# Optimization experiments

Hardware: AMD Instinct MI355X
Metric: run time of the kernel (lower is better)

## Reference

```python
import math
import jax, jax.numpy as jnp
import numpy as np

FILTER_ORDER = 64
FILTER_EMB_DIM = 5
HIDDEN = 256
SHIFT = 0.05
FAST_DECAY_PCT = 0.3
SLOW_DECAY_PCT = 1.5
TARGET = 0.01


def setup_inputs() -> dict:
    key = jax.random.key(0)
    ks = jax.random.split(key, 8)
    B, C, L = 8, HIDDEN, 8192

    def lin_w(k, fan_out, fan_in):
        return jax.random.normal(k, (fan_out, fan_in), jnp.float32) / np.sqrt(fan_in).astype(np.float32)

    return {
        "x": jax.random.normal(ks[0], (B, C, L), jnp.float32),
        "W1": lin_w(ks[1], FILTER_ORDER, FILTER_EMB_DIM),
        "b1": jnp.zeros((FILTER_ORDER,), jnp.float32),
        "freq0": jnp.ones((1, FILTER_ORDER), jnp.float32),
        "W2": lin_w(ks[2], FILTER_ORDER, FILTER_ORDER),
        "b2": jnp.zeros((FILTER_ORDER,), jnp.float32),
        "freq1": jnp.ones((1, FILTER_ORDER), jnp.float32),
        "W3": lin_w(ks[3], FILTER_ORDER, FILTER_ORDER),
        "b3": jnp.zeros((FILTER_ORDER,), jnp.float32),
        "freq2": jnp.ones((1, FILTER_ORDER), jnp.float32),
        "Wout": lin_w(ks[4], HIDDEN, FILTER_ORDER),
        "D": jax.random.normal(ks[5], (HIDDEN,), jnp.float32),
        "L": L,
    }


def _pos_emb(L):
    # HyenaDnaPositionalEmbedding: z (1, L, emb_dim), t (1, L, 1)
    t = jnp.linspace(0.0, 1.0, L, dtype=jnp.float32)[None, :, None]
    t_rescaled = jnp.linspace(0.0, L - 1, L, dtype=jnp.float32)[None, :, None]
    w = 2.0 * math.pi * t_rescaled / L  # (1, L, 1)
    bands = (FILTER_EMB_DIM - 1) // 2
    f = jnp.linspace(1e-4, bands - 1, bands, dtype=jnp.float32)[None, None]  # (1, 1, bands)
    z = jnp.concatenate([t, jnp.cos(-f * w), jnp.sin(-f * w)], axis=-1)  # (1, L, emb_dim)
    return z, t


def _filter_kernel(W1, b1, freq0, W2, b2, freq1, W3, b3, freq2, Wout, L):
    z, t = _pos_emb(L)
    h = jnp.sin(freq0 * (jnp.einsum('ble,oe->blo', z, W1) + b1))
    h = jnp.sin(freq1 * (jnp.einsum('blo,po->blp', h, W2) + b2))
    h = jnp.sin(freq2 * (jnp.einsum('blo,po->blp', h, W3) + b3))
    h = jnp.einsum('blo,do->bld', h, Wout)  # (1, L, HIDDEN)
    # exponential modulation window
    max_decay = math.log(TARGET) / FAST_DECAY_PCT
    min_decay = math.log(TARGET) / SLOW_DECAY_PCT
    deltas = jnp.linspace(min_decay, max_decay, HIDDEN, dtype=jnp.float32)[None, None]
    decay = jnp.exp(-t * jnp.abs(deltas))  # (1, L, HIDDEN)
    h = h * (decay + SHIFT)
    return h[0].T  # (HIDDEN, L) channels-major kernel


def _fftconv(u, k, D):
    # y = conv(u, k) + u * D via FFT, zero-padded to 2L (linear convolution)
    L = u.shape[-1]
    fft_size = 2 * L
    k_f = jnp.fft.rfft(k.astype(jnp.float32), n=fft_size) / fft_size  # (C, fft_size//2+1)
    u_f = jnp.fft.rfft(u.astype(jnp.float32), n=fft_size)             # (B, C, fft_size//2+1)
    y = jnp.fft.irfft(u_f * k_f, n=fft_size, norm='forward')[..., :L]
    return (y + u * D[:, None]).astype(u.dtype)


def reference(x, W1, b1, freq0, W2, b2, freq1, W3, b3, freq2, Wout, D, L):
    k = _filter_kernel(W1, b1, freq0, W2, b2, freq1, W3, b3, freq2, Wout, L)
    return _fftconv(x, k, D)
```

## Files before the change

### kernel.cpp

```cpp
#include <hip/hip_runtime.h>

#define L_SEQ 8192
#define NTH 512
#define HID 256
#define PIDX(i) ((i) + ((i) >> 4))
#define LDS_SZ 8704

#define ANG16 3.83495196971410315e-4f
#define ANG8  7.66990393942820630e-4f
#define CS16 0.99999992646571789f
#define SN16 3.83495187571395563e-4f
#define CS8  0.99999970586287223f
#define SN8  7.66990318742704490e-4f
#define C707 0.70710678118654752f

__device__ float2 TWID[4088];
template<int M> struct TWOFF;
template<> struct TWOFF<512> { static constexpr int v = 0;    };
template<> struct TWOFF<64>  { static constexpr int v = 3584; };
template<> struct TWOFF<8>   { static constexpr int v = 4032; };

__global__ void twid_kernel() {
  int i = threadIdx.x;
  #pragma unroll
  for (int j = 1; j <= 7; ++j) {
    float s, c;
    sincosf(-6.2831853071795864769f * (float)(i*j) / 4096.0f, &s, &c);
    TWID[i*7 + j-1] = make_float2(c, s);
  }
  if (i < 64) {
    #pragma unroll
    for (int j = 1; j <= 7; ++j) {
      float s, c;
      sincosf(-6.2831853071795864769f * (float)(i*j) / 512.0f, &s, &c);
      TWID[3584 + i*7 + j-1] = make_float2(c, s);
    }
  }
  if (i < 8) {
    #pragma unroll
    for (int j = 1; j <= 7; ++j) {
      float s, c;
      sincosf(-6.2831853071795864769f * (float)(i*j) / 64.0f, &s, &c);
      TWID[4032 + i*7 + j-1] = make_float2(c, s);
    }
  }
}

__device__ __forceinline__ float2 cmul(float2 a, float2 b) {
  return make_float2(a.x*b.x - a.y*b.y, a.x*b.y + a.y*b.x);
}
__device__ __forceinline__ float2 cadd(float2 a, float2 b){ return make_float2(a.x+b.x, a.y+b.y); }
__device__ __forceinline__ float2 csub(float2 a, float2 b){ return make_float2(a.x-b.x, a.y-b.y); }

__device__ __forceinline__ void bf4_fwd(float2 a0, float2 a1, float2 a2, float2 a3,
                                        float2& o0, float2& o1, float2& o2, float2& o3) {
  float2 t0 = cadd(a0,a2), t1 = csub(a0,a2), t2 = cadd(a1,a3), t3 = csub(a1,a3);
  o0 = cadd(t0,t2);
  o2 = csub(t0,t2);
  o1 = make_float2(t1.x + t3.y, t1.y - t3.x);
  o3 = make_float2(t1.x - t3.y, t1.y + t3.x);
}
__device__ __forceinline__ void bf4_inv(float2 c0, float2 c1, float2 c2, float2 c3,
                                        float2& o0, float2& o1, float2& o2, float2& o3) {
  float2 u0 = cadd(c0,c2), u2 = csub(c0,c2), u1 = cadd(c1,c3);
  float2 v3 = make_float2(c3.y - c1.y, c1.x - c3.x);
  o0 = cadd(u0,u1); o2 = csub(u0,u1); o1 = cadd(u2,v3); o3 = csub(u2,v3);
}

__device__ __forceinline__ void fwd8(float2 P[8]) {
  float2 e0=cadd(P[0],P[4]), e1=cadd(P[1],P[5]), e2=cadd(P[2],P[6]), e3=cadd(P[3],P[7]);
  float2 o0=csub(P[0],P[4]), o1=csub(P[1],P[5]), o2=csub(P[2],P[6]), o3=csub(P[3],P[7]);
  o1 = make_float2((o1.x+o1.y)*C707, (o1.y-o1.x)*C707);
  o2 = make_float2(o2.y, -o2.x);
  o3 = make_float2((o3.y-o3.x)*C707, -(o3.x+o3.y)*C707);
  float2 q0,q1,q2,q3;
  bf4_fwd(e0,e1,e2,e3,q0,q1,q2,q3);
  P[0]=q0; P[2]=q1; P[4]=q2; P[6]=q3;
  bf4_fwd(o0,o1,o2,o3,q0,q1,q2,q3);
  P[1]=q0; P[3]=q1; P[5]=q2; P[7]=q3;
}
__device__ __forceinline__ void inv8(float2 P[8]) {
  float2 E0,E1,E2,E3,O0,O1,O2,O3;
  bf4_inv(P[0],P[2],P[4],P[6],E0,E1,E2,E3);
  bf4_inv(P[1],P[3],P[5],P[7],O0,O1,O2,O3);
  O1 = make_float2((O1.x-O1.y)*C707, (O1.x+O1.y)*C707);
  O2 = make_float2(-O2.y, O2.x);
  O3 = make_float2(-(O3.x+O3.y)*C707, (O3.x-O3.y)*C707);
  P[0]=cadd(E0,O0); P[4]=csub(E0,O0);
  P[1]=cadd(E1,O1); P[5]=csub(E1,O1);
  P[2]=cadd(E2,O2); P[6]=csub(E2,O2);
  P[3]=cadd(E3,O3); P[7]=csub(E3,O3);
}

template<int M>
__device__ __forceinline__ void fwd_stage8_2(float2* __restrict__ X0,
                                             float2* __restrict__ X1, int t) {
  #pragma unroll
  for (int r = 0; r < 2; ++r) {
    int s = t + NTH*r;
    int i2 = s & (M-1);
    int g  = s / M;
    int base = g*8*M + i2;
    const float2* __restrict__ wp = TWID + TWOFF<M>::v + i2*7;
    float2 w[7];
    #pragma unroll
    for (int j=0;j<7;++j) w[j] = wp[j];
    float2 Pa[8], Pb[8];
    #pragma unroll
    for (int j=0;j<8;++j) { Pa[j] = X0[PIDX(base + j*M)]; Pb[j] = X1[PIDX(base + j*M)]; }
    fwd8(Pa); fwd8(Pb);
    X0[PIDX(base)] = Pa[0];
    X1[PIDX(base)] = Pb[0];
    #pragma unroll
    for (int j=1;j<8;++j) {
      X0[PIDX(base + j*M)] = cmul(Pa[j], w[j-1]);
      X1[PIDX(base + j*M)] = cmul(Pb[j], w[j-1]);
    }
  }
}
template<int M>
__device__ __forceinline__ void inv_stage8_2(float2* __restrict__ X0,
                                             float2* __restrict__ X1, int t) {
  #pragma unroll
  for (int r = 0; r < 2; ++r) {
    int s = t + NTH*r;
    int i2 = s & (M-1);
    int g  = s / M;
    int base = g*8*M + i2;
    const float2* __restrict__ wp = TWID + TWOFF<M>::v + i2*7;
    float2 w[7];
    #pragma unroll
    for (int j=0;j<7;++j) { float2 v = wp[j]; w[j] = make_float2(v.x, -v.y); }
    float2 Pa[8], Pb[8];
    Pa[0] = X0[PIDX(base)];
    Pb[0] = X1[PIDX(base)];
    #pragma unroll
    for (int j=1;j<8;++j) {
      Pa[j] = cmul(X0[PIDX(base + j*M)], w[j-1]);
      Pb[j] = cmul(X1[PIDX(base + j*M)], w[j-1]);
    }
    inv8(Pa); inv8(Pb);
    #pragma unroll
    for (int j=0;j<8;++j) {
      X0[PIDX(base + j*M)] = Pa[j];
      X1[PIDX(base + j*M)] = Pb[j];
    }
  }
}

__device__ __forceinline__ void fft_mid_fwd2(float2* __restrict__ X0,
                                             float2* __restrict__ X1, int t) {
  __syncthreads();
  fwd_stage8_2<512>(X0,X1,t); __syncthreads();
  fwd_stage8_2<64>(X0,X1,t);  __syncthreads();
  fwd_stage8_2<8>(X0,X1,t);   __syncthreads();
}
__device__ __forceinline__ void fft_mid_inv2(float2* __restrict__ X0,
                                             float2* __restrict__ X1, int t) {
  __syncthreads();
  inv_stage8_2<8>(X0,X1,t);   __syncthreads();
  inv_stage8_2<64>(X0,X1,t);  __syncthreads();
  inv_stage8_2<512>(X0,X1,t); __syncthreads();
}

__device__ __forceinline__ void middle_pointwise2(float2* __restrict__ X0,
                                                  float2* __restrict__ X1,
                                                  const float2* __restrict__ K, int t) {
  #pragma unroll
  for (int r = 0; r < 2; ++r) {
    int base = 8*(t + NTH*r);
    float2 kreg[8];
    #pragma unroll
    for (int q=0;q<8;++q) kreg[q] = K[base+q];
    float2 Pa[8], Pb[8];
    #pragma unroll
    for (int q=0;q<8;++q) { Pa[q] = X0[PIDX(base+q)]; Pb[q] = X1[PIDX(base+q)]; }
    fwd8(Pa); fwd8(Pb);
    #pragma unroll
    for (int q=0;q<8;++q) { Pa[q] = cmul(Pa[q], kreg[q]); Pb[q] = cmul(Pb[q], kreg[q]); }
    inv8(Pa); inv8(Pb);
    #pragma unroll
    for (int q=0;q<8;++q) { X0[PIDX(base+q)] = Pa[q]; X1[PIDX(base+q)] = Pb[q]; }
  }
}

__global__ __launch_bounds__(256) void mlp_kernel(
    const float* __restrict__ W1, const float* __restrict__ b1, const float* __restrict__ fq0,
    const float* __restrict__ W2, const float* __restrict__ b2, const float* __restrict__ fq1,
    const float* __restrict__ W3, const float* __restrict__ b3, const float* __restrict__ fq2,
    float* __restrict__ h3g) {
  __shared__ float hs[2][16][64];
  int tid = threadIdx.x;
  int lane = tid & 63, w = tid >> 6;
  int l0 = blockIdx.x * 16;

  float w1r[5];
  #pragma unroll
  for (int e = 0; e < 5; ++e) w1r[e] = W1[lane*5+e];
  float b1v = b1[lane], f0 = fq0[lane];
  #pragma unroll
  for (int r = 0; r < 4; ++r) {
    int l = l0 + w + 4*r;
    float t = (float)l * (1.0f / (float)(L_SEQ - 1));
    float ang = 6.2831853071795864769f * (float)l / (float)L_SEQ;
    float s0, c0, s1, c1;
    __sincosf(1e-4f * ang, &s0, &c0);
    __sincosf(ang, &s1, &c1);
    float acc = b1v + t*w1r[0] + c0*w1r[1] + c1*w1r[2] - s0*w1r[3] - s1*w1r[4];
    hs[0][w + 4*r][lane] = __sinf(f0 * acc);
  }
  __syncthreads();

  float wr[64];
  #pragma unroll
  for (int j = 0; j < 16; ++j) *(float4*)&wr[4*j] = *(const float4*)&W2[lane*64 + 4*j];
  float b2v = b2[lane], f1 = fq1[lane];
  #pragma unroll
  for (int r = 0; r < 4; ++r) {
    int ll = w + 4*r;
    float a0 = 0.f, a1 = 0.f, a2 = 0.f, a3 = 0.f;
    #pragma unroll
    for (int o = 0; o < 64; o += 4) {
      a0 += hs[0][ll][o+0] * wr[o+0];
      a1 += hs[0][ll][o+1] * wr[o+1];
      a2 += hs[0][ll][o+2] * wr[o+2];
      a3 += hs[0][ll][o+3] * wr[o+3];
    }
    hs[1][ll][lane] = __sinf(f1 * (b2v + ((a0+a1)+(a2+a3))));
  }
  __syncthreads();

  #pragma unroll
  for (int j = 0; j < 16; ++j) *(float4*)&wr[4*j] = *(const float4*)&W3[lane*64 + 4*j];
  float b3v = b3[lane], f2 = fq2[lane];
  #pragma unroll
  for (int r = 0; r < 4; ++r) {
    int ll = w + 4*r;
    float a0 = 0.f, a1 = 0.f, a2 = 0.f, a3 = 0.f;
    #pragma unroll
    for (int o = 0; o < 64; o += 4) {
      a0 += hs[1][ll][o+0] * wr[o+0];
      a1 += hs[1][ll][o+1] * wr[o+1];
      a2 += hs[1][ll][o+2] * wr[o+2];
      a3 += hs[1][ll][o+3] * wr[o+3];
    }
    h3g[(size_t)(l0 + ll) * 64 + lane] = __sinf(f2 * (b3v + ((a0+a1)+(a2+a3))));
  }
}

__global__ __launch_bounds__(256) void kwrite_kernel(const float* __restrict__ h3g,
                                                     const float* __restrict__ Wout,
                                                     const float* __restrict__ Dv,
                                                     float* __restrict__ kbuf) {
  __shared__ float tileh[256][65];
  int tid = threadIdx.x;
  int l0 = blockIdx.x * 256;
  int c0 = blockIdx.y * 32;
  {
    const float4* src = (const float4*)(h3g + (size_t)l0 * 64);
    #pragma unroll
    for (int q = 0; q < 16; ++q) {
      int idx = tid + 256*q;
      int row = idx >> 4, col4 = idx & 15;
      float4 v = src[idx];
      tileh[row][col4*4+0] = v.x;
      tileh[row][col4*4+1] = v.y;
      tileh[row][col4*4+2] = v.z;
      tileh[row][col4*4+3] = v.w;
    }
  }
  __syncthreads();
  float hr[64];
  #pragma unroll
  for (int o = 0; o < 64; ++o) hr[o] = tileh[tid][o];
  int l = l0 + tid;
  float t = (float)l * (1.0f / (float)(L_SEQ - 1));
  const float mind = -3.0701134573253945f;
  const float maxd = -15.350567286626972f;
  for (int jj = 0; jj < 32; ++jj) {
    int c = c0 + jj;
    float a0 = 0.f, a1 = 0.f, a2 = 0.f, a3 = 0.f;
    #pragma unroll
    for (int o = 0; o < 64; o += 4) {
      a0 += hr[o+0] * Wout[c*64+o+0];
      a1 += hr[o+1] * Wout[c*64+o+1];
      a2 += hr[o+2] * Wout[c*64+o+2];
      a3 += hr[o+3] * Wout[c*64+o+3];
    }
    float acc = (a0+a1)+(a2+a3);
    float delta = mind + (maxd - mind) * ((float)c * (1.0f/255.0f));
    float dec = __expf(-t * fabsf(delta)) + 0.05f;
    float v = acc * dec;
    if (l == 0) v += Dv[c];
    kbuf[(size_t)c * L_SEQ + l] = v;
  }
}

__global__ __launch_bounds__(NTH) void kf_kernel(const float* __restrict__ kbuf,
                                                 float2* __restrict__ Kf) {
  __shared__ float2 X0[LDS_SZ];
  __shared__ float2 X1[LDS_SZ];
  int c = blockIdx.x;
  int t = threadIdx.x;
  const float* kr = kbuf + (size_t)c * L_SEQ;
  const float sc = 1.0f / 16384.0f;
  #pragma unroll
  for (int r = 0; r < 2; ++r) {
    int n0 = 4*t + 2048*r;
    float4 lo4 = *(const float4*)(kr + n0);
    float4 hi4 = *(const float4*)(kr + n0 + 4096);
    float s8, c8;  __sincosf(-ANG8  * (float)n0, &s8, &c8);
    float s16, c16; __sincosf(-ANG16 * (float)n0, &s16, &c16);
    float2 w8  = make_float2(c8, s8);
    float2 w16 = make_float2(c16, s16);
    #pragma unroll
    for (int j = 0; j < 4; ++j) {
      if (j) { w8 = cmul(w8, make_float2(CS8, -SN8)); w16 = cmul(w16, make_float2(CS16, -SN16)); }
      float klo = ((const float*)&lo4)[j];
      float khi = ((const float*)&hi4)[j];
      X0[PIDX(n0+j)]      = make_float2(klo + khi, 0.f);
      float d = klo - khi;
      X0[PIDX(n0+j+4096)] = make_float2(d * w8.x, d * w8.y);
      float2 vlo = make_float2(klo * w16.x, klo * w16.y);
      float2 vhi = make_float2(khi * w16.y, -khi * w16.x);
      float2 w8x = cmul(w16, w16);
      X1[PIDX(n0+j)]      = cadd(vlo, vhi);
      X1[PIDX(n0+j+4096)] = cmul(csub(vlo, vhi), w8x);
    }
  }
  fft_mid_fwd2(X0, X1, t);
  #pragma unroll
  for (int r = 0; r < 2; ++r) {
    int base = 8*(t + NTH*r);
    float2 P0[8], P1[8];
    #pragma unroll
    for (int q=0;q<8;++q) { P0[q] = X0[PIDX(base+q)]; P1[q] = X1[PIDX(base+q)]; }
    fwd8(P0); fwd8(P1);
    float2* out0 = Kf + (size_t)c * 16384 + base;
    float2* out1 = out0 + 8192;
    #pragma unroll
    for (int q=0;q<8;++q) {
      out0[q] = make_float2(P0[q].x*sc, P0[q].y*sc);
      out1[q] = make_float2(P1[q].x*sc, P1[q].y*sc);
    }
  }
}

__global__ __launch_bounds__(NTH) void conv_kernel(const float* __restrict__ x,
                                                   const float2* __restrict__ Kf,
                                                   float* __restrict__ y) {
  __shared__ float2 X0[LDS_SZ];
  __shared__ float2 X1[LDS_SZ];
  int c = blockIdx.x;
  int p = blockIdx.y;
  int t = threadIdx.x;
  const float* u00 = x + ((size_t)(p)     * HID + c) * L_SEQ;
  const float* u01 = x + ((size_t)(p + 4) * HID + c) * L_SEQ;
  const float* u10 = x + ((size_t)(p + 2) * HID + c) * L_SEQ;
  const float* u11 = x + ((size_t)(p + 6) * HID + c) * L_SEQ;
  const float2* KA = Kf + (size_t)c * 16384;
  const float2* KB = KA + 8192;
  float* y00 = y + ((size_t)(p)     * HID + c) * L_SEQ;
  float* y01 = y + ((size_t)(p + 4) * HID + c) * L_SEQ;
  float* y10 = y + ((size_t)(p + 2) * HID + c) * L_SEQ;
  float* y11 = y + ((size_t)(p + 6) * HID + c) * L_SEQ;

  #pragma unroll
  for (int r = 0; r < 2; ++r) {
    int n0 = 4*t + 2048*r;
    float4 a00 = *(const float4*)(u00 + n0);
    float4 a01 = *(const float4*)(u01 + n0);
    float4 b00 = *(const float4*)(u00 + n0 + 4096);
    float4 b01 = *(const float4*)(u01 + n0 + 4096);
    float4 a10 = *(const float4*)(u10 + n0);
    float4 a11 = *(const float4*)(u11 + n0);
    float4 b10 = *(const float4*)(u10 + n0 + 4096);
    float4 b11 = *(const float4*)(u11 + n0 + 4096);
    float sb, cb; __sincosf(-ANG16 * (float)n0, &sb, &cb);
    float2 w16 = make_float2(cb, sb);
    #pragma unroll
    for (int j = 0; j < 4; ++j) {
      if (j) w16 = cmul(w16, make_float2(CS16, -SN16));
      float2 wmi = make_float2(w16.y, -w16.x);
      float2 w8 = cmul(w16, w16);
      {
        float2 vlo = cmul(make_float2(((const float*)&a00)[j], ((const float*)&a01)[j]), w16);
        float2 vhi = cmul(make_float2(((const float*)&b00)[j], ((const float*)&b01)[j]), wmi);
        X0[PIDX(n0+j)]      = cadd(vlo, vhi);
        X0[PIDX(n0+j+4096)] = cmul(csub(vlo, vhi), w8);
      }
      {
        float2 vlo = cmul(make_float2(((const float*)&a10)[j], ((const float*)&a11)[j]), w16);
        float2 vhi = cmul(make_float2(((const float*)&b10)[j], ((const float*)&b11)[j]), wmi);
        X1[PIDX(n0+j)]      = cadd(vlo, vhi);
        X1[PIDX(n0+j+4096)] = cmul(csub(vlo, vhi), w8);
      }
    }
  }
  fft_mid_fwd2(X0, X1, t);
  middle_pointwise2(X0, X1, KB, t);
  fft_mid_inv2(X0, X1, t);
  float2 st0[16], st1[16];
  #pragma unroll
  for (int r = 0; r < 2; ++r) {
    int n0 = 4*t + 2048*r;
    float sb, cb; __sincosf(ANG16 * (float)n0, &sb, &cb);
    float2 w16b = make_float2(cb, sb);
    #pragma unroll
    for (int j = 0; j < 4; ++j) {
      if (j) w16b = cmul(w16b, make_float2(CS16, SN16));
      float2 w8b = cmul(w16b, w16b);
      float2 wib = make_float2(-w16b.y, w16b.x);
      {
        float2 P = X0[PIDX(n0+j)], Q = X0[PIDX(n0+j+4096)];
        float2 tt = cmul(Q, w8b);
        st0[r*4+j]     = cmul(cadd(P, tt), w16b);
        st0[8 + r*4+j] = cmul(csub(P, tt), wib);
      }
      {
        float2 P = X1[PIDX(n0+j)], Q = X1[PIDX(n0+j+4096)];
        float2 tt = cmul(Q, w8b);
        st1[r*4+j]     = cmul(cadd(P, tt), w16b);
        st1[8 + r*4+j] = cmul(csub(P, tt), wib);
      }
    }
  }
  __syncthreads();

  #pragma unroll
  for (int r = 0; r < 2; ++r) {
    int n0 = 4*t + 2048*r;
    float4 a00 = *(const float4*)(u00 + n0);
    float4 a01 = *(const float4*)(u01 + n0);
    float4 b00 = *(const float4*)(u00 + n0 + 4096);
    float4 b01 = *(const float4*)(u01 + n0 + 4096);
    float4 a10 = *(const float4*)(u10 + n0);
    float4 a11 = *(const float4*)(u11 + n0);
    float4 b10 = *(const float4*)(u10 + n0 + 4096);
    float4 b11 = *(const float4*)(u11 + n0 + 4096);
    float sb, cb; __sincosf(-ANG8 * (float)n0, &sb, &cb);
    float2 w8 = make_float2(cb, sb);
    #pragma unroll
    for (int j = 0; j < 4; ++j) {
      if (j) w8 = cmul(w8, make_float2(CS8, -SN8));
      {
        float2 vlo = make_float2(((const float*)&a00)[j], ((const float*)&a01)[j]);
        float2 vhi = make_float2(((const float*)&b00)[j], ((const float*)&b01)[j]);
        X0[PIDX(n0+j)]      = cadd(vlo, vhi);
        X0[PIDX(n0+j+4096)] = cmul(csub(vlo, vhi), w8);
      }
      {
        float2 vlo = make_float2(((const float*)&a10)[j], ((const float*)&a11)[j]);
        float2 vhi = make_float2(((const float*)&b10)[j], ((const float*)&b11)[j]);
        X1[PIDX(n0+j)]      = cadd(vlo, vhi);
        X1[PIDX(n0+j+4096)] = cmul(csub(vlo, vhi), w8);
      }
    }
  }
  fft_mid_fwd2(X0, X1, t);
  middle_pointwise2(X0, X1, KA, t);
  fft_mid_inv2(X0, X1, t);
  #pragma unroll
  for (int r = 0; r < 2; ++r) {
    int n0 = 4*t + 2048*r;
    float sb, cb; __sincosf(ANG8 * (float)n0, &sb, &cb);
    float2 w8b0 = make_float2(cb, sb);
    {
      float2 w8b = w8b0;
      float4 w00, w01, w10, w11;
      #pragma unroll
      for (int j = 0; j < 4; ++j) {
        if (j) w8b = cmul(w8b, make_float2(CS8, SN8));
        float2 P = X0[PIDX(n0+j)], Q = X0[PIDX(n0+j+4096)];
        float2 tt = cmul(Q, w8b);
        float2 lo = cadd(cadd(P, tt), st0[r*4+j]);
        float2 hi = cadd(csub(P, tt), st0[8 + r*4+j]);
        ((float*)&w00)[j] = lo.x; ((float*)&w01)[j] = lo.y;
        ((float*)&w10)[j] = hi.x; ((float*)&w11)[j] = hi.y;
      }
      *(float4*)(y00 + n0)        = w00;
      *(float4*)(y01 + n0)        = w01;
      *(float4*)(y00 + n0 + 4096) = w10;
      *(float4*)(y01 + n0 + 4096) = w11;
    }
    {
      float2 w8b = w8b0;
      float4 w00, w01, w10, w11;
      #pragma unroll
      for (int j = 0; j < 4; ++j) {
        if (j) w8b = cmul(w8b, make_float2(CS8, SN8));
        float2 P = X1[PIDX(n0+j)], Q = X1[PIDX(n0+j+4096)];
        float2 tt = cmul(Q, w8b);
        float2 lo = cadd(cadd(P, tt), st1[r*4+j]);
        float2 hi = cadd(csub(P, tt), st1[8 + r*4+j]);
        ((float*)&w00)[j] = lo.x; ((float*)&w01)[j] = lo.y;
        ((float*)&w10)[j] = hi.x; ((float*)&w11)[j] = hi.y;
      }
      *(float4*)(y10 + n0)        = w00;
      *(float4*)(y11 + n0)        = w01;
      *(float4*)(y10 + n0 + 4096) = w10;
      *(float4*)(y11 + n0 + 4096) = w11;
    }
  }
}

extern "C" void kernel_launch(void* const* d_in, const int* in_sizes, int n_in,
                              void* d_out, int out_size, void* d_ws, size_t ws_size,
                              hipStream_t stream) {
  const float* x    = (const float*)d_in[0];
  const float* W1   = (const float*)d_in[1];
  const float* b1   = (const float*)d_in[2];
  const float* fq0  = (const float*)d_in[3];
  const float* W2   = (const float*)d_in[4];
  const float* b2   = (const float*)d_in[5];
  const float* fq1  = (const float*)d_in[6];
  const float* W3   = (const float*)d_in[7];
  const float* b3   = (const float*)d_in[8];
  const float* fq2  = (const float*)d_in[9];
  const float* Wout = (const float*)d_in[10];
  const float* Dv   = (const float*)d_in[11];

  float*  kbuf = (float*)d_ws;
  float2* Kf   = (float2*)((char*)d_ws + (size_t)HID * L_SEQ * sizeof(float));
  float*  h3g  = (float*)((char*)d_ws + 38ull*1024*1024);
  float*  y    = (float*)d_out;

  twid_kernel  <<<dim3(1),     512, 0, stream>>>();
  mlp_kernel   <<<dim3(512),   256, 0, stream>>>(W1,b1,fq0,W2,b2,fq1,W3,b3,fq2,h3g);
  kwrite_kernel<<<dim3(32, 8), 256, 0, stream>>>(h3g, Wout, Dv, kbuf);
  kf_kernel    <<<dim3(256),    NTH, 0, stream>>>(kbuf, Kf);
  conv_kernel  <<<dim3(256, 2), NTH, 0, stream>>>(x, Kf, y);
}
```

Measured before the change: 164.7 us.

## Restructure conv FFT so each block handles one batch pair in a single pass

The conv kernel previously computed two half-spectrum passes (even/odd via KB then KA), each over two batch pairs, and kept staged results in registers across a barrier. Now each block processes one packed batch pair once: X0 holds the even-decimated half and X1 the twisted odd half, and they are multiplied by KA and KB respectively and recombined in a single epilogue. The grid doubles in y to keep total work covered. This drops a second global read of x, an extra FFT round-trip per block and large register staging. It also simplifies twiddle generation in kf_kernel. In exchange each block does less work and the block count doubles.

```diff
diff --git a/kernel.cpp b/kernel.cpp
--- a/kernel.cpp
+++ b/kernel.cpp
@@ -165,19 +165,20 @@
 
 __device__ __forceinline__ void middle_pointwise2(float2* __restrict__ X0,
                                                   float2* __restrict__ X1,
-                                                  const float2* __restrict__ K, int t) {
+                                                  const float2* __restrict__ KA,
+                                                  const float2* __restrict__ KB, int t) {
   #pragma unroll
   for (int r = 0; r < 2; ++r) {
     int base = 8*(t + NTH*r);
-    float2 kreg[8];
-    #pragma unroll
-    for (int q=0;q<8;++q) kreg[q] = K[base+q];
+    float2 ka[8], kb[8];
+    #pragma unroll
+    for (int q=0;q<8;++q) { ka[q] = KA[base+q]; kb[q] = KB[base+q]; }
     float2 Pa[8], Pb[8];
     #pragma unroll
     for (int q=0;q<8;++q) { Pa[q] = X0[PIDX(base+q)]; Pb[q] = X1[PIDX(base+q)]; }
     fwd8(Pa); fwd8(Pb);
     #pragma unroll
-    for (int q=0;q<8;++q) { Pa[q] = cmul(Pa[q], kreg[q]); Pb[q] = cmul(Pb[q], kreg[q]); }
+    for (int q=0;q<8;++q) { Pa[q] = cmul(Pa[q], ka[q]); Pb[q] = cmul(Pb[q], kb[q]); }
     inv8(Pa); inv8(Pb);
     #pragma unroll
     for (int q=0;q<8;++q) { X0[PIDX(base+q)] = Pa[q]; X1[PIDX(base+q)] = Pb[q]; }
@@ -309,13 +310,12 @@
     int n0 = 4*t + 2048*r;
     float4 lo4 = *(const float4*)(kr + n0);
     float4 hi4 = *(const float4*)(kr + n0 + 4096);
-    float s8, c8;  __sincosf(-ANG8  * (float)n0, &s8, &c8);
     float s16, c16; __sincosf(-ANG16 * (float)n0, &s16, &c16);
-    float2 w8  = make_float2(c8, s8);
     float2 w16 = make_float2(c16, s16);
     #pragma unroll
     for (int j = 0; j < 4; ++j) {
-      if (j) { w8 = cmul(w8, make_float2(CS8, -SN8)); w16 = cmul(w16, make_float2(CS16, -SN16)); }
+      if (j) w16 = cmul(w16, make_float2(CS16, -SN16));
+      float2 w8 = cmul(w16, w16);
       float klo = ((const float*)&lo4)[j];
       float khi = ((const float*)&hi4)[j];
       X0[PIDX(n0+j)]      = make_float2(klo + khi, 0.f);
@@ -323,9 +323,8 @@
       X0[PIDX(n0+j+4096)] = make_float2(d * w8.x, d * w8.y);
       float2 vlo = make_float2(klo * w16.x, klo * w16.y);
       float2 vhi = make_float2(khi * w16.y, -khi * w16.x);
-      float2 w8x = cmul(w16, w16);
       X1[PIDX(n0+j)]      = cadd(vlo, vhi);
-      X1[PIDX(n0+j+4096)] = cmul(csub(vlo, vhi), w8x);
+      X1[PIDX(n0+j+4096)] = cmul(csub(vlo, vhi), w8);
     }
   }
   fft_mid_fwd2(X0, X1, t);
@@ -354,153 +353,62 @@
   int c = blockIdx.x;
   int p = blockIdx.y;
   int t = threadIdx.x;
-  const float* u00 = x + ((size_t)(p)     * HID + c) * L_SEQ;
-  const float* u01 = x + ((size_t)(p + 4) * HID + c) * L_SEQ;
-  const float* u10 = x + ((size_t)(p + 2) * HID + c) * L_SEQ;
-  const float* u11 = x + ((size_t)(p + 6) * HID + c) * L_SEQ;
+  const float* u0 = x + ((size_t)p       * HID + c) * L_SEQ;
+  const float* u1 = x + ((size_t)(p + 4) * HID + c) * L_SEQ;
   const float2* KA = Kf + (size_t)c * 16384;
   const float2* KB = KA + 8192;
-  float* y00 = y + ((size_t)(p)     * HID + c) * L_SEQ;
-  float* y01 = y + ((size_t)(p + 4) * HID + c) * L_SEQ;
-  float* y10 = y + ((size_t)(p + 2) * HID + c) * L_SEQ;
-  float* y11 = y + ((size_t)(p + 6) * HID + c) * L_SEQ;
+  float* y0 = y + ((size_t)p       * HID + c) * L_SEQ;
+  float* y1 = y + ((size_t)(p + 4) * HID + c) * L_SEQ;
 
   #pragma unroll
   for (int r = 0; r < 2; ++r) {
     int n0 = 4*t + 2048*r;
-    float4 a00 = *(const float4*)(u00 + n0);
-    float4 a01 = *(const float4*)(u01 + n0);
-    float4 b00 = *(const float4*)(u00 + n0 + 4096);
-    float4 b01 = *(const float4*)(u01 + n0 + 4096);
-    float4 a10 = *(const float4*)(u10 + n0);
-    float4 a11 = *(const float4*)(u11 + n0);
-    float4 b10 = *(const float4*)(u10 + n0 + 4096);
-    float4 b11 = *(const float4*)(u11 + n0 + 4096);
+    float4 a0 = *(const float4*)(u0 + n0);
+    float4 a1 = *(const float4*)(u1 + n0);
+    float4 b0 = *(const float4*)(u0 + n0 + 4096);
+    float4 b1 = *(const float4*)(u1 + n0 + 4096);
     float sb, cb; __sincosf(-ANG16 * (float)n0, &sb, &cb);
     float2 w16 = make_float2(cb, sb);
     #pragma unroll
     for (int j = 0; j < 4; ++j) {
       if (j) w16 = cmul(w16, make_float2(CS16, -SN16));
-      float2 wmi = make_float2(w16.y, -w16.x);
       float2 w8 = cmul(w16, w16);
-      {
-        float2 vlo = cmul(make_float2(((const float*)&a00)[j], ((const float*)&a01)[j]), w16);
-        float2 vhi = cmul(make_float2(((const float*)&b00)[j], ((const float*)&b01)[j]), wmi);
-        X0[PIDX(n0+j)]      = cadd(vlo, vhi);
-        X0[PIDX(n0+j+4096)] = cmul(csub(vlo, vhi), w8);
-      }
-      {
-        float2 vlo = cmul(make_float2(((const float*)&a10)[j], ((const float*)&a11)[j]), w16);
-        float2 vhi = cmul(make_float2(((const float*)&b10)[j], ((const float*)&b11)[j]), wmi);
-        X1[PIDX(n0+j)]      = cadd(vlo, vhi);
-        X1[PIDX(n0+j+4096)] = cmul(csub(vlo, vhi), w8);
-      }
+      float2 vlo = make_float2(((const float*)&a0)[j], ((const float*)&a1)[j]);
+      float2 vhi = make_float2(((const float*)&b0)[j], ((const float*)&b1)[j]);
+      X0[PIDX(n0+j)]      = cadd(vlo, vhi);
+      X0[PIDX(n0+j+4096)] = cmul(csub(vlo, vhi), w8);
+      float2 vloB = cmul(vlo, w16);
+      float2 vhiB = cmul(vhi, make_float2(w16.y, -w16.x));
+      X1[PIDX(n0+j)]      = cadd(vloB, vhiB);
+      X1[PIDX(n0+j+4096)] = cmul(csub(vloB, vhiB), w8);
     }
   }
   fft_mid_fwd2(X0, X1, t);
-  middle_pointwise2(X0, X1, KB, t);
+  middle_pointwise2(X0, X1, KA, KB, t);
   fft_mid_inv2(X0, X1, t);
-  float2 st0[16], st1[16];
   #pragma unroll
   for (int r = 0; r < 2; ++r) {
     int n0 = 4*t + 2048*r;
     float sb, cb; __sincosf(ANG16 * (float)n0, &sb, &cb);
     float2 w16b = make_float2(cb, sb);
+    float4 w00, w01, w10, w11;
     #pragma unroll
     for (int j = 0; j < 4; ++j) {
       if (j) w16b = cmul(w16b, make_float2(CS16, SN16));
       float2 w8b = cmul(w16b, w16b);
-      float2 wib = make_float2(-w16b.y, w16b.x);
-      {
-        float2 P = X0[PIDX(n0+j)], Q = X0[PIDX(n0+j+4096)];
-        float2 tt = cmul(Q, w8b);
-        st0[r*4+j]     = cmul(cadd(P, tt), w16b);
-        st0[8 + r*4+j] = cmul(csub(P, tt), wib);
-      }
-      {
-        float2 P = X1[PIDX(n0+j)], Q = X1[PIDX(n0+j+4096)];
-        float2 tt = cmul(Q, w8b);
-        st1[r*4+j]     = cmul(cadd(P, tt), w16b);
-        st1[8 + r*4+j] = cmul(csub(P, tt), wib);
-      }
-    }
-  }
-  __syncthreads();
-
-  #pragma unroll
-  for (int r = 0; r < 2; ++r) {
-    int n0 = 4*t + 2048*r;
-    float4 a00 = *(const float4*)(u00 + n0);
-    float4 a01 = *(const float4*)(u01 + n0);
-    float4 b00 = *(const float4*)(u00 + n0 + 4096);
-    float4 b01 = *(const float4*)(u01 + n0 + 4096);
-    float4 a10 = *(const float4*)(u10 + n0);
-    float4 a11 = *(const float4*)(u11 + n0);
-    float4 b10 = *(const float4*)(u10 + n0 + 4096);
-    float4 b11 = *(const float4*)(u11 + n0 + 4096);
-    float sb, cb; __sincosf(-ANG8 * (float)n0, &sb, &cb);
-    float2 w8 = make_float2(cb, sb);
-    #pragma unroll
-    for (int j = 0; j < 4; ++j) {
-      if (j) w8 = cmul(w8, make_float2(CS8, -SN8));
-      {
-        float2 vlo = make_float2(((const float*)&a00)[j], ((const float*)&a01)[j]);
-        float2 vhi = make_float2(((const float*)&b00)[j], ((const float*)&b01)[j]);
-        X0[PIDX(n0+j)]      = cadd(vlo, vhi);
-        X0[PIDX(n0+j+4096)] = cmul(csub(vlo, vhi), w8);
-      }
-      {
-        float2 vlo = make_float2(((const float*)&a10)[j], ((const float*)&a11)[j]);
-        float2 vhi = make_float2(((const float*)&b10)[j], ((const float*)&b11)[j]);
-        X1[PIDX(n0+j)]      = cadd(vlo, vhi);
-        X1[PIDX(n0+j+4096)] = cmul(csub(vlo, vhi), w8);
-      }
-    }
-  }
-  fft_mid_fwd2(X0, X1, t);
-  middle_pointwise2(X0, X1, KA, t);
-  fft_mid_inv2(X0, X1, t);
-  #pragma unroll
-  for (int r = 0; r < 2; ++r) {
-    int n0 = 4*t + 2048*r;
-    float sb, cb; __sincosf(ANG8 * (float)n0, &sb, &cb);
-    float2 w8b0 = make_float2(cb, sb);
-    {
-      float2 w8b = w8b0;
-      float4 w00, w01, w10, w11;
-      #pragma unroll
-      for (int j = 0; j < 4; ++j) {
-        if (j) w8b = cmul(w8b, make_float2(CS8, SN8));
-        float2 P = X0[PIDX(n0+j)], Q = X0[PIDX(n0+j+4096)];
-        float2 tt = cmul(Q, w8b);
-        float2 lo = cadd(cadd(P, tt), st0[r*4+j]);
-        float2 hi = cadd(csub(P, tt), st0[8 + r*4+j]);
-        ((float*)&w00)[j] = lo.x; ((float*)&w01)[j] = lo.y;
-        ((float*)&w10)[j] = hi.x; ((float*)&w11)[j] = hi.y;
-      }
-      *(float4*)(y00 + n0)        = w00;
-      *(float4*)(y01 + n0)        = w01;
-      *(float4*)(y00 + n0 + 4096) = w10;
-      *(float4*)(y01 + n0 + 4096) = w11;
-    }
-    {
-      float2 w8b = w8b0;
-      float4 w00, w01, w10, w11;
-      #pragma unroll
-      for (int j = 0; j < 4; ++j) {
-        if (j) w8b = cmul(w8b, make_float2(CS8, SN8));
-        float2 P = X1[PIDX(n0+j)], Q = X1[PIDX(n0+j+4096)];
-        float2 tt = cmul(Q, w8b);
-        float2 lo = cadd(cadd(P, tt), st1[r*4+j]);
-        float2 hi = cadd(csub(P, tt), st1[8 + r*4+j]);
-        ((float*)&w00)[j] = lo.x; ((float*)&w01)[j] = lo.y;
-        ((float*)&w10)[j] = hi.x; ((float*)&w11)[j] = hi.y;
-      }
-      *(float4*)(y10 + n0)        = w00;
-      *(float4*)(y11 + n0)        = w01;
-      *(float4*)(y10 + n0 + 4096) = w10;
-      *(float4*)(y11 + n0 + 4096) = w11;
-    }
+      float2 P0 = X0[PIDX(n0+j)], Q0 = X0[PIDX(n0+j+4096)];
+      float2 P1 = X1[PIDX(n0+j)], Q1 = X1[PIDX(n0+j+4096)];
+      float2 tt0 = cmul(Q0, w8b);
+      float2 tt1 = cmul(Q1, w8b);
+      float2 lo = cadd(cadd(P0, tt0), cmul(cadd(P1, tt1), w16b));
+      float2 hi = cadd(csub(P0, tt0), cmul(csub(P1, tt1), make_float2(-w16b.y, w16b.x)));
+      ((float*)&w00)[j] = lo.x; ((float*)&w01)[j] = lo.y;
+      ((float*)&w10)[j] = hi.x; ((float*)&w11)[j] = hi.y;
+    }
+    *(float4*)(y0 + n0)        = w00;
+    *(float4*)(y1 + n0)        = w01;
+    *(float4*)(y0 + n0 + 4096) = w10;
+    *(float4*)(y1 + n0 + 4096) = w11;
   }
 }
 
@@ -529,5 +437,5 @@
   mlp_kernel   <<<dim3(512),   256, 0, stream>>>(W1,b1,fq0,W2,b2,fq1,W3,b3,fq2,h3g);
   kwrite_kernel<<<dim3(32, 8), 256, 0, stream>>>(h3g, Wout, Dv, kbuf);
   kf_kernel    <<<dim3(256),    NTH, 0, stream>>>(kbuf, Kf);
-  conv_kernel  <<<dim3(256, 2), NTH, 0, stream>>>(x, Kf, y);
-}
+  conv_kernel  <<<dim3(256, 4), NTH, 0, stream>>>(x, Kf, y);
+}
```

Result: faster. 150.7 us (-8.5%).
